# Kernel tuning notes

Measured on AMD Instinct MI355X. Metric: run time of the kernel, lower is better.

Reference implementation:

```python
import jax, jax.numpy as jnp
import numpy as np

D_MODEL = 512
D_STATE = 64
DT = 1.0
BATCH = 8
SEQ = 4096


def setup_inputs() -> dict:
    key = jax.random.key(0)
    ks = jax.random.split(key, 5)
    u = jax.random.normal(ks[0], (BATCH, SEQ, D_MODEL), dtype=jnp.float32)
    log_A_real = jnp.zeros((D_STATE,), dtype=jnp.float32)
    log_A_imag = 0.1 * jax.random.normal(ks[1], (D_STATE,), dtype=jnp.float32)
    B_w = 0.1 * jax.random.normal(ks[2], (2 * D_STATE, D_MODEL), dtype=jnp.float32)
    C_w = 0.1 * jax.random.normal(ks[3], (D_MODEL, 2 * D_STATE), dtype=jnp.float32)
    D_w = jnp.eye(D_MODEL, dtype=jnp.float32)
    return {"u": u, "log_A_real": log_A_real, "log_A_imag": log_A_imag,
            "B_w": B_w, "C_w": C_w, "D_w": D_w}


def reference(u, log_A_real, log_A_imag, B_w, C_w, D_w):
    # Bilinear discretization of diagonal A_c = -exp(log_A_real) + i*log_A_imag
    ar = -jnp.exp(log_A_real)
    ai = log_A_imag
    h = 0.5 * DT
    nr, ni = 1.0 + h * ar, h * ai          # numerator 1 + dt/2 * A
    dr, di = 1.0 - h * ar, -h * ai          # denominator 1 - dt/2 * A
    den = dr * dr + di * di
    Ar = (nr * dr + ni * di) / den          # Re(A_bar), shape (N,)
    Ai = (ni * dr - nr * di) / den          # Im(A_bar)

    N = log_A_real.shape[0]
    Bu = jnp.einsum('btd,nd->btn', u, B_w)  # (B, T, 2N)
    bu_re = jnp.swapaxes(Bu[..., :N], 0, 1)  # (T, B, N)
    bu_im = jnp.swapaxes(Bu[..., N:], 0, 1)

    batch = u.shape[0]
    h0 = (jnp.zeros((batch, N), u.dtype), jnp.zeros((batch, N), u.dtype))

    def step(carry, x):
        hr, hi = carry
        xr, xi = x
        nhr = Ar * hr - Ai * hi + xr        # complex multiply + add, real form
        nhi = Ar * hi + Ai * hr + xi
        return (nhr, nhi), (nhr, nhi)

    _, (hr_all, hi_all) = jax.lax.scan(step, h0, (bu_re, bu_im))
    h_cat = jnp.concatenate([hr_all, hi_all], axis=-1)   # (T, B, 2N)
    y = jnp.einsum('tbn,dn->btd', h_cat, C_w) + jnp.einsum('btd,ed->bte', u, D_w)
    return y
```

## Files before the change

### kernel.cpp

```cpp
#include <hip/hip_runtime.h>
#include <hip/hip_bf16.h>


#define D_MODEL 512
#define NSTATE  64
#define N2      128
#define BATCH   8
#define SEQ     4096
#define MTOT    (BATCH*SEQ)
#define LC      16
#define NC      (SEQ/LC)

#define OFFB_ABAR   0u
#define OFFB_POWTAB 512u
#define OFFB_BWPB   16384u
#define OFFB_W2B    147456u
#define OFFB_BU     1048576u
#define OFFB_E      17825792u
#define OFFB_P      18874368u

typedef __bf16  bf16x8  __attribute__((ext_vector_type(8)));
typedef float   f32x4   __attribute__((ext_vector_type(4)));
typedef unsigned short ushort8 __attribute__((ext_vector_type(8)));

__device__ __forceinline__ unsigned short f2bf(float f) {
    union { float f; unsigned int u; } v; v.f = f;
    unsigned int r = v.u + 0x7fffu + ((v.u >> 16) & 1u);
    return (unsigned short)(r >> 16);
}

__device__ __forceinline__ void gload_lds16(const void* g, void* l) {
    __builtin_amdgcn_global_load_lds(
        (const __attribute__((address_space(1))) void*)g,
        (__attribute__((address_space(3))) void*)l, 16, 0, 0);
}

__global__ __launch_bounds__(256) void prep_kernel(
    const float* __restrict__ lar, const float* __restrict__ lai,
    const float* __restrict__ Bw,  const float* __restrict__ Cw,
    const float* __restrict__ Dw,
    float* __restrict__ abar, float* __restrict__ powtab,
    unsigned short* __restrict__ Bwpb, unsigned short* __restrict__ W2b)
{
    int tid = blockIdx.x * blockDim.x + threadIdx.x;
    if (blockIdx.x == 0 && threadIdx.x < 64) {
        int n = threadIdx.x;
        float ar = -expf(lar[n]);
        float ai = lai[n];
        const float h = 0.5f;
        float nr = 1.f + h * ar, ni = h * ai;
        float dr = 1.f - h * ar, di = -h * ai;
        float den = dr * dr + di * di;
        float Ar = (nr * dr + ni * di) / den;
        float Ai = (ni * dr - nr * di) / den;
        abar[2 * n] = Ar; abar[2 * n + 1] = Ai;
        float pr = Ar, pi = Ai;
        for (int i = 0; i < LC; ++i) {
            powtab[(i * 64 + n) * 2]     = pr;
            powtab[(i * 64 + n) * 2 + 1] = pi;
            float npr = pr * Ar - pi * Ai;
            float npi = pr * Ai + pi * Ar;
            pr = npr; pi = npi;
        }
    }
    int stride = gridDim.x * blockDim.x;
    for (int idx = tid; idx < N2 * D_MODEL; idx += stride) {
        int np = idx / D_MODEL, k = idx % D_MODEL;
        int src = (np & 1) ? (64 + (np >> 1)) : (np >> 1);
        Bwpb[idx] = f2bf(Bw[src * D_MODEL + k]);
    }
    for (int idx = tid; idx < D_MODEL * 640; idx += stride) {
        int d = idx / 640, k = idx % 640;
        float v;
        if (k < D_MODEL) v = Dw[d * D_MODEL + k];
        else {
            int np = k - D_MODEL;
            int src = (np & 1) ? (64 + (np >> 1)) : (np >> 1);
            v = Cw[d * N2 + src];
        }
        W2b[idx] = f2bf(v);
    }
}

__global__ __launch_bounds__(256) void gemm_bf16_kernel(
    const float* __restrict__ A1, int lda1, int K1,
    const float* __restrict__ A2, int lda2, int K2,
    const unsigned short* __restrict__ W, int ldb,
    float* __restrict__ C, int ldc)
{
    __shared__ __align__(16) unsigned short As[128 * 64];
    __shared__ __align__(16) unsigned short Bs[128 * 64];
    const int tid  = threadIdx.x;
    const int lane = tid & 63;
    const int w    = tid >> 6;
    const int wm   = (w >> 1) * 64;
    const int wn   = (w & 1) * 64;
    const int m0   = blockIdx.x * 128;
    const int n0   = blockIdx.y * 128;

    f32x4 acc[4][4];
#pragma unroll
    for (int i = 0; i < 4; ++i)
#pragma unroll
        for (int j = 0; j < 4; ++j)
            acc[i][j] = (f32x4){0.f, 0.f, 0.f, 0.f};

    const int Ktot = K1 + K2;
    const int tr = tid >> 3;
    const int tc = tid & 7;

    for (int k0 = 0; k0 < Ktot; k0 += 64) {
        __syncthreads();
#pragma unroll
        for (int q = 0; q < 4; ++q) {
            int r = q * 32 + tr;
            int cs = tc ^ (r & 7);
            gload_lds16(W + (size_t)(n0 + r) * ldb + k0 + cs * 8,
                        (char*)Bs + (q * 256 + tid) * 16);
        }
        const float* Ab; int lda_; int kk0;
        if (k0 < K1) { Ab = A1; lda_ = lda1; kk0 = k0; }
        else         { Ab = A2; lda_ = lda2; kk0 = k0 - K1; }
#pragma unroll
        for (int q = 0; q < 4; ++q) {
            int r = q * 32 + tr;
            const float* src = Ab + (size_t)(m0 + r) * lda_ + kk0 + tc * 8;
            float4 v0 = *(const float4*)src;
            float4 v1 = *(const float4*)(src + 4);
            ushort8 p;
            p[0] = f2bf(v0.x); p[1] = f2bf(v0.y); p[2] = f2bf(v0.z); p[3] = f2bf(v0.w);
            p[4] = f2bf(v1.x); p[5] = f2bf(v1.y); p[6] = f2bf(v1.z); p[7] = f2bf(v1.w);
            int cd = tc ^ (r & 7);
            *(ushort8*)((char*)As + r * 128 + cd * 16) = p;
        }
        __syncthreads();

#pragma unroll
        for (int kk = 0; kk < 2; ++kk) {
            bf16x8 a[4], b[4];
#pragma unroll
            for (int i = 0; i < 4; ++i) {
                int row = wm + i * 16 + (lane & 15);
                int kb  = kk * 64 + ((lane >> 4) << 4);
                a[i] = *(const bf16x8*)((const char*)As + row * 128 + (kb ^ ((row & 7) << 4)));
            }
#pragma unroll
            for (int j = 0; j < 4; ++j) {
                int row = wn + j * 16 + (lane & 15);
                int kb  = kk * 64 + ((lane >> 4) << 4);
                b[j] = *(const bf16x8*)((const char*)Bs + row * 128 + (kb ^ ((row & 7) << 4)));
            }
#pragma unroll
            for (int i = 0; i < 4; ++i)
#pragma unroll
                for (int j = 0; j < 4; ++j)
                    acc[i][j] = __builtin_amdgcn_mfma_f32_16x16x32_bf16(a[i], b[j], acc[i][j], 0, 0, 0);
        }
    }

#pragma unroll
    for (int i = 0; i < 4; ++i)
#pragma unroll
        for (int j = 0; j < 4; ++j) {
            int col = n0 + wn + j * 16 + (lane & 15);
#pragma unroll
            for (int r = 0; r < 4; ++r) {
                int row = m0 + wm + i * 16 + ((lane >> 4) << 2) + r;
                C[(size_t)row * ldc + col] = acc[i][j][r];
            }
        }
}

__global__ __launch_bounds__(64) void scan_local_kernel(
    float* Bu, const float* __restrict__ abar, float* __restrict__ E)
{
    int n = threadIdx.x;
    int bx = blockIdx.x;
    int b = bx >> 8, c = bx & (NC - 1);
    float Ar = abar[2 * n], Ai = abar[2 * n + 1];
    float hr = 0.f, hi = 0.f;
    size_t base = (size_t)(b * SEQ + c * LC) * N2 + 2 * n;
#pragma unroll
    for (int i = 0; i < LC; ++i) {
        float2 x = *(const float2*)&Bu[base + (size_t)i * N2];
        float nhr = fmaf(Ar, hr, fmaf(-Ai, hi, x.x));
        float nhi = fmaf(Ar, hi, fmaf(Ai, hr, x.y));
        hr = nhr; hi = nhi;
        *(float2*)&Bu[base + (size_t)i * N2] = make_float2(hr, hi);
    }
    *(float2*)&E[((b * NC + c) * 64 + n) * 2] = make_float2(hr, hi);
}

__global__ __launch_bounds__(64) void scan_carry_kernel(
    const float* __restrict__ E, const float* __restrict__ powtab,
    float* __restrict__ P)
{
    int n = threadIdx.x;
    int b = blockIdx.x;
    float aLr = powtab[((LC - 1) * 64 + n) * 2];
    float aLi = powtab[((LC - 1) * 64 + n) * 2 + 1];
    float pr = 0.f, pi = 0.f;
    for (int c = 0; c < NC; ++c) {
        int idx = ((b * NC + c) * 64 + n) * 2;
        P[idx] = pr; P[idx + 1] = pi;
        float2 e = *(const float2*)&E[idx];
        float npr = fmaf(aLr, pr, fmaf(-aLi, pi, e.x));
        float npi = fmaf(aLr, pi, fmaf(aLi, pr, e.y));
        pr = npr; pi = npi;
    }
}

__global__ __launch_bounds__(64) void scan_fix_kernel(
    float* Bu, const float* __restrict__ P, const float* __restrict__ powtab)
{
    int n = threadIdx.x;
    int bx = blockIdx.x;
    int b = bx >> 8, c = bx & (NC - 1);
    if (c == 0) return;
    float2 p = *(const float2*)&P[((b * NC + c) * 64 + n) * 2];
    size_t base = (size_t)(b * SEQ + c * LC) * N2 + 2 * n;
#pragma unroll
    for (int i = 0; i < LC; ++i) {
        float2 wv = *(const float2*)&powtab[(i * 64 + n) * 2];
        float cr = wv.x * p.x - wv.y * p.y;
        float ci = fmaf(wv.x, p.y, wv.y * p.x);
        float2 hcur = *(const float2*)&Bu[base + (size_t)i * N2];
        hcur.x += cr; hcur.y += ci;
        *(float2*)&Bu[base + (size_t)i * N2] = hcur;
    }
}

extern "C" void kernel_launch(void* const* d_in, const int* in_sizes, int n_in,
                              void* d_out, int out_size, void* d_ws, size_t ws_size,
                              hipStream_t stream)
{
    const float* u   = (const float*)d_in[0];
    const float* lar = (const float*)d_in[1];
    const float* lai = (const float*)d_in[2];
    const float* Bw  = (const float*)d_in[3];
    const float* Cw  = (const float*)d_in[4];
    const float* Dw  = (const float*)d_in[5];
    float* y = (float*)d_out;
    char* ws = (char*)d_ws;

    float*          abar   = (float*)(ws + OFFB_ABAR);
    float*          powtab = (float*)(ws + OFFB_POWTAB);
    unsigned short* Bwpb   = (unsigned short*)(ws + OFFB_BWPB);
    unsigned short* W2b    = (unsigned short*)(ws + OFFB_W2B);
    float*          Bu     = (float*)(ws + OFFB_BU);
    float*          E      = (float*)(ws + OFFB_E);
    float*          P      = (float*)(ws + OFFB_P);

    hipLaunchKernelGGL(prep_kernel, dim3(128), dim3(256), 0, stream,
                       lar, lai, Bw, Cw, Dw, abar, powtab, Bwpb, W2b);
    hipLaunchKernelGGL(gemm_bf16_kernel, dim3(MTOT / 128, 1), dim3(256), 0, stream,
                       u, D_MODEL, D_MODEL, u, 0, 0, Bwpb, D_MODEL, Bu, N2);
    hipLaunchKernelGGL(scan_local_kernel, dim3(BATCH * NC), dim3(64), 0, stream,
                       Bu, abar, E);
    hipLaunchKernelGGL(scan_carry_kernel, dim3(BATCH), dim3(64), 0, stream,
                       E, powtab, P);
    hipLaunchKernelGGL(scan_fix_kernel, dim3(BATCH * NC), dim3(64), 0, stream,
                       Bu, P, powtab);
    hipLaunchKernelGGL(gemm_bf16_kernel, dim3(MTOT / 128, D_MODEL / 128), dim3(256), 0, stream,
                       u, D_MODEL, D_MODEL, Bu, N2, N2, W2b, 640, y, D_MODEL);
}
```

Before: 202.8 us.

## Fuse local scan into first GEMM, parallelize carry scan, apply fix in second GEMM

The first GEMM now computes Bu per 64-row tile, runs the 16-step local chunk scan in shared memory, and writes the local states as bf16 plus per-chunk end states. The carry scan is parallelized with a wave-level shuffle prefix scan over chunks instead of a serial loop. The carry correction (powtab times P) is applied inside the second GEMM's A-tile load, so the separate scan_local and scan_fix passes over the full fp32 Bu buffer go away. When the workspace is large enough, a bf16 copy of u is also cached so the second GEMM can load it directly with global-to-LDS copies instead of converting it again; this adds extra writes in the first GEMM and stores the local states in bf16.

```diff
diff --git a/kernel.cpp b/kernel.cpp
--- a/kernel.cpp
+++ b/kernel.cpp
@@ -3,21 +3,23 @@
 
 
 #define D_MODEL 512
-#define NSTATE  64
 #define N2      128
 #define BATCH   8
 #define SEQ     4096
 #define MTOT    (BATCH*SEQ)
 #define LC      16
 #define NC      (SEQ/LC)
+#define PADW    132
 
 #define OFFB_ABAR   0u
 #define OFFB_POWTAB 512u
 #define OFFB_BWPB   16384u
 #define OFFB_W2B    147456u
-#define OFFB_BU     1048576u
-#define OFFB_E      17825792u
-#define OFFB_P      18874368u
+#define OFFB_E      1048576u
+#define OFFB_P      2097152u
+#define OFFB_HLOC   3145728u
+#define OFFB_UBF    11534336u
+#define WS_NEED_UBF 45088768u
 
 typedef __bf16  bf16x8  __attribute__((ext_vector_type(8)));
 typedef float   f32x4   __attribute__((ext_vector_type(4)));
@@ -28,7 +30,10 @@
     unsigned int r = v.u + 0x7fffu + ((v.u >> 16) & 1u);
     return (unsigned short)(r >> 16);
 }
-
+__device__ __forceinline__ float bf2f(unsigned short s) {
+    union { unsigned int u; float f; } v; v.u = ((unsigned int)s) << 16;
+    return v.f;
+}
 __device__ __forceinline__ void gload_lds16(const void* g, void* l) {
     __builtin_amdgcn_global_load_lds(
         (const __attribute__((address_space(1))) void*)g,
@@ -56,8 +61,8 @@
         abar[2 * n] = Ar; abar[2 * n + 1] = Ai;
         float pr = Ar, pi = Ai;
         for (int i = 0; i < LC; ++i) {
-            powtab[(i * 64 + n) * 2]     = pr;
-            powtab[(i * 64 + n) * 2 + 1] = pi;
+            powtab[i * 128 + 2 * n]     = pr;
+            powtab[i * 128 + 2 * n + 1] = pi;
             float npr = pr * Ar - pi * Ai;
             float npi = pr * Ai + pi * Ar;
             pr = npr; pi = npi;
@@ -82,11 +87,193 @@
     }
 }
 
-__global__ __launch_bounds__(256) void gemm_bf16_kernel(
-    const float* __restrict__ A1, int lda1, int K1,
-    const float* __restrict__ A2, int lda2, int K2,
-    const unsigned short* __restrict__ W, int ldb,
-    float* __restrict__ C, int ldc)
+__global__ __launch_bounds__(256) void gemm1_fused(
+    const float* __restrict__ u, const unsigned short* __restrict__ Bwpb,
+    const float* __restrict__ abar,
+    unsigned short* __restrict__ Hloc, float* __restrict__ E,
+    unsigned short* __restrict__ u_bf, int write_ubf)
+{
+    __shared__ __align__(16) unsigned short As[64 * 64];
+    __shared__ __align__(16) unsigned short Bs[128 * 64];
+    __shared__ __align__(16) float Hs[64 * PADW];
+    const int tid  = threadIdx.x;
+    const int lane = tid & 63;
+    const int w    = tid >> 6;
+    const int wm   = (w >> 1) * 32;
+    const int wn   = (w & 1) * 64;
+    const int m0   = blockIdx.x * 64;
+
+    f32x4 acc[2][4];
+#pragma unroll
+    for (int i = 0; i < 2; ++i)
+#pragma unroll
+        for (int j = 0; j < 4; ++j)
+            acc[i][j] = (f32x4){0.f, 0.f, 0.f, 0.f};
+
+    const int tr = tid >> 3, tc = tid & 7;
+
+    for (int k0 = 0; k0 < D_MODEL; k0 += 64) {
+        __syncthreads();
+#pragma unroll
+        for (int q = 0; q < 4; ++q) {
+            int r = q * 32 + tr;
+            int cs = tc ^ (r & 7);
+            gload_lds16(Bwpb + (size_t)r * D_MODEL + k0 + cs * 8,
+                        (char*)Bs + (q * 256 + tid) * 16);
+        }
+#pragma unroll
+        for (int q = 0; q < 2; ++q) {
+            int r = q * 32 + tr;
+            const float* src = u + (size_t)(m0 + r) * D_MODEL + k0 + tc * 8;
+            float4 v0 = *(const float4*)src;
+            float4 v1 = *(const float4*)(src + 4);
+            ushort8 p;
+            p[0] = f2bf(v0.x); p[1] = f2bf(v0.y); p[2] = f2bf(v0.z); p[3] = f2bf(v0.w);
+            p[4] = f2bf(v1.x); p[5] = f2bf(v1.y); p[6] = f2bf(v1.z); p[7] = f2bf(v1.w);
+            int cd = tc ^ (r & 7);
+            *(ushort8*)((char*)As + r * 128 + cd * 16) = p;
+            if (write_ubf)
+                *(ushort8*)&u_bf[(size_t)(m0 + r) * D_MODEL + k0 + tc * 8] = p;
+        }
+        __syncthreads();
+#pragma unroll
+        for (int kk = 0; kk < 2; ++kk) {
+            bf16x8 a[2], b[4];
+#pragma unroll
+            for (int i = 0; i < 2; ++i) {
+                int row = wm + i * 16 + (lane & 15);
+                int kb  = kk * 64 + ((lane >> 4) << 4);
+                a[i] = *(const bf16x8*)((const char*)As + row * 128 + (kb ^ ((row & 7) << 4)));
+            }
+#pragma unroll
+            for (int j = 0; j < 4; ++j) {
+                int row = wn + j * 16 + (lane & 15);
+                int kb  = kk * 64 + ((lane >> 4) << 4);
+                b[j] = *(const bf16x8*)((const char*)Bs + row * 128 + (kb ^ ((row & 7) << 4)));
+            }
+#pragma unroll
+            for (int i = 0; i < 2; ++i)
+#pragma unroll
+                for (int j = 0; j < 4; ++j)
+                    acc[i][j] = __builtin_amdgcn_mfma_f32_16x16x32_bf16(a[i], b[j], acc[i][j], 0, 0, 0);
+        }
+    }
+
+#pragma unroll
+    for (int i = 0; i < 2; ++i)
+#pragma unroll
+        for (int j = 0; j < 4; ++j) {
+            int col = wn + j * 16 + (lane & 15);
+#pragma unroll
+            for (int r = 0; r < 4; ++r) {
+                int row = wm + i * 16 + ((lane >> 4) << 2) + r;
+                Hs[row * PADW + col] = acc[i][j][r];
+            }
+        }
+    __syncthreads();
+
+    {
+        int n  = tid & 63;
+        int cl = tid >> 6;
+        float2 ab = *(const float2*)&abar[2 * n];
+        float hr = 0.f, hi = 0.f;
+#pragma unroll
+        for (int i = 0; i < LC; ++i) {
+            int t = cl * LC + i;
+            float xr = Hs[t * PADW + 2 * n];
+            float xi = Hs[t * PADW + 2 * n + 1];
+            float nhr = fmaf(ab.x, hr, fmaf(-ab.y, hi, xr));
+            float nhi = fmaf(ab.x, hi, fmaf(ab.y, hr, xi));
+            hr = nhr; hi = nhi;
+            Hs[t * PADW + 2 * n]     = hr;
+            Hs[t * PADW + 2 * n + 1] = hi;
+        }
+        int b  = m0 >> 12;
+        int c0 = (m0 & 4095) >> 4;
+        *(float2*)&E[((size_t)(b * 64 + n) * NC + c0 + cl) * 2] = make_float2(hr, hi);
+    }
+    __syncthreads();
+
+#pragma unroll
+    for (int q = 0; q < 2; ++q) {
+        int r = q * 32 + tr;
+        int cb = tc * 16;
+        const float* row = &Hs[r * PADW + cb];
+        ushort8 o0, o1;
+#pragma unroll
+        for (int j = 0; j < 8; ++j) o0[j] = f2bf(row[j]);
+#pragma unroll
+        for (int j = 0; j < 8; ++j) o1[j] = f2bf(row[8 + j]);
+        *(ushort8*)&Hloc[(size_t)(m0 + r) * N2 + cb]     = o0;
+        *(ushort8*)&Hloc[(size_t)(m0 + r) * N2 + cb + 8] = o1;
+    }
+}
+
+__global__ __launch_bounds__(256) void scan_carry_par(
+    const float* __restrict__ E, const float* __restrict__ abar,
+    float* __restrict__ P)
+{
+    const int b    = blockIdx.x;
+    const int wv   = threadIdx.x >> 6;
+    const int lane = threadIdx.x & 63;
+
+    for (int n = wv * 16; n < wv * 16 + 16; ++n) {
+        float2 ab = *(const float2*)&abar[2 * n];
+        float ar = ab.x, ai = ab.y;
+        for (int k = 0; k < 4; ++k) {
+            float t = ar * ar - ai * ai;  ai = 2.f * ar * ai;  ar = t;
+        }
+        float pr[7], pi[7];
+        pr[0] = ar; pi[0] = ai;
+#pragma unroll
+        for (int k = 1; k < 7; ++k) {
+            pr[k] = pr[k-1] * pr[k-1] - pi[k-1] * pi[k-1];
+            pi[k] = 2.f * pr[k-1] * pi[k-1];
+        }
+        int L = lane + 1;
+        float wr = 1.f, wi = 0.f;
+#pragma unroll
+        for (int k = 0; k < 7; ++k) if ((L >> k) & 1) {
+            float t = wr * pr[k] - wi * pi[k];
+            wi = wr * pi[k] + wi * pr[k]; wr = t;
+        }
+        const float* Eb = E + (size_t)(b * 64 + n) * NC * 2;
+        float cr = 0.f, ci = 0.f;
+        for (int s = 0; s < 4; ++s) {
+            float2 e = *(const float2*)&Eb[(s * 64 + lane) * 2];
+            float xr = e.x, xi = e.y;
+#pragma unroll
+            for (int k = 0; k < 6; ++k) {
+                int d = 1 << k;
+                float tr_ = __shfl_up(xr, (unsigned)d);
+                float ti_ = __shfl_up(xi, (unsigned)d);
+                if (lane >= d) {
+                    xr = fmaf(pr[k], tr_, fmaf(-pi[k], ti_, xr));
+                    xi = fmaf(pr[k], ti_, fmaf(pi[k], tr_, xi));
+                }
+            }
+            float gr = fmaf(wr, cr, fmaf(-wi, ci, xr));
+            float gi = fmaf(wr, ci, fmaf(wi, cr, xi));
+            float exr = __shfl_up(gr, 1u);
+            float exi = __shfl_up(gi, 1u);
+            if (lane == 0) { exr = cr; exi = ci; }
+            *(float2*)&P[(size_t)(b * NC + s * 64 + lane) * N2 + 2 * n] =
+                make_float2(exr, exi);
+            cr = __shfl(gr, 63);
+            ci = __shfl(gi, 63);
+        }
+    }
+}
+
+template<bool A1BF>
+__global__ __launch_bounds__(256) void gemm2_fused(
+    const float* __restrict__ uf,
+    const unsigned short* __restrict__ ubf,
+    const unsigned short* __restrict__ Hloc,
+    const unsigned short* __restrict__ W2b,
+    const float* __restrict__ P,
+    const float* __restrict__ powtab,
+    float* __restrict__ y)
 {
     __shared__ __align__(16) unsigned short As[128 * 64];
     __shared__ __align__(16) unsigned short Bs[128 * 64];
@@ -105,36 +292,69 @@
         for (int j = 0; j < 4; ++j)
             acc[i][j] = (f32x4){0.f, 0.f, 0.f, 0.f};
 
-    const int Ktot = K1 + K2;
-    const int tr = tid >> 3;
-    const int tc = tid & 7;
-
-    for (int k0 = 0; k0 < Ktot; k0 += 64) {
+    const int tr = tid >> 3, tc = tid & 7;
+
+    for (int k0 = 0; k0 < 640; k0 += 64) {
         __syncthreads();
 #pragma unroll
         for (int q = 0; q < 4; ++q) {
             int r = q * 32 + tr;
             int cs = tc ^ (r & 7);
-            gload_lds16(W + (size_t)(n0 + r) * ldb + k0 + cs * 8,
+            gload_lds16(W2b + (size_t)(n0 + r) * 640 + k0 + cs * 8,
                         (char*)Bs + (q * 256 + tid) * 16);
         }
-        const float* Ab; int lda_; int kk0;
-        if (k0 < K1) { Ab = A1; lda_ = lda1; kk0 = k0; }
-        else         { Ab = A2; lda_ = lda2; kk0 = k0 - K1; }
-#pragma unroll
-        for (int q = 0; q < 4; ++q) {
-            int r = q * 32 + tr;
-            const float* src = Ab + (size_t)(m0 + r) * lda_ + kk0 + tc * 8;
-            float4 v0 = *(const float4*)src;
-            float4 v1 = *(const float4*)(src + 4);
-            ushort8 p;
-            p[0] = f2bf(v0.x); p[1] = f2bf(v0.y); p[2] = f2bf(v0.z); p[3] = f2bf(v0.w);
-            p[4] = f2bf(v1.x); p[5] = f2bf(v1.y); p[6] = f2bf(v1.z); p[7] = f2bf(v1.w);
-            int cd = tc ^ (r & 7);
-            *(ushort8*)((char*)As + r * 128 + cd * 16) = p;
+        if (k0 < D_MODEL) {
+            if constexpr (A1BF) {
+#pragma unroll
+                for (int q = 0; q < 4; ++q) {
+                    int r = q * 32 + tr;
+                    int cs = tc ^ (r & 7);
+                    gload_lds16(ubf + (size_t)(m0 + r) * D_MODEL + k0 + cs * 8,
+                                (char*)As + (q * 256 + tid) * 16);
+                }
+            } else {
+#pragma unroll
+                for (int q = 0; q < 4; ++q) {
+                    int r = q * 32 + tr;
+                    const float* src = uf + (size_t)(m0 + r) * D_MODEL + k0 + tc * 8;
+                    float4 v0 = *(const float4*)src;
+                    float4 v1 = *(const float4*)(src + 4);
+                    ushort8 p;
+                    p[0] = f2bf(v0.x); p[1] = f2bf(v0.y); p[2] = f2bf(v0.z); p[3] = f2bf(v0.w);
+                    p[4] = f2bf(v1.x); p[5] = f2bf(v1.y); p[6] = f2bf(v1.z); p[7] = f2bf(v1.w);
+                    int cd = tc ^ (r & 7);
+                    *(ushort8*)((char*)As + r * 128 + cd * 16) = p;
+                }
+            }
+        } else {
+            const int kk0 = k0 - D_MODEL;
+#pragma unroll
+            for (int q = 0; q < 4; ++q) {
+                int r = q * 32 + tr;
+                int m = m0 + r;
+                int b = m >> 12, t = m & 4095;
+                int c = t >> 4, i = t & 15;
+                ushort8 hl = *(const ushort8*)&Hloc[(size_t)m * N2 + kk0 + tc * 8];
+                const float* Pp = P + (size_t)(b * NC + c) * N2 + kk0 + tc * 8;
+                float4 p0 = *(const float4*)Pp;
+                float4 p1 = *(const float4*)(Pp + 4);
+                const float* Wp = powtab + i * 128 + kk0 + tc * 8;
+                float4 w0 = *(const float4*)Wp;
+                float4 w1 = *(const float4*)(Wp + 4);
+                ushort8 p;
+                p[0] = f2bf(fmaf(w0.x, p0.x, fmaf(-w0.y, p0.y, bf2f(hl[0]))));
+                p[1] = f2bf(fmaf(w0.x, p0.y, fmaf( w0.y, p0.x, bf2f(hl[1]))));
+                p[2] = f2bf(fmaf(w0.z, p0.z, fmaf(-w0.w, p0.w, bf2f(hl[2]))));
+                p[3] = f2bf(fmaf(w0.z, p0.w, fmaf( w0.w, p0.z, bf2f(hl[3]))));
+                p[4] = f2bf(fmaf(w1.x, p1.x, fmaf(-w1.y, p1.y, bf2f(hl[4]))));
+                p[5] = f2bf(fmaf(w1.x, p1.y, fmaf( w1.y, p1.x, bf2f(hl[5]))));
+                p[6] = f2bf(fmaf(w1.z, p1.z, fmaf(-w1.w, p1.w, bf2f(hl[6]))));
+                p[7] = f2bf(fmaf(w1.z, p1.w, fmaf( w1.w, p1.z, bf2f(hl[7]))));
+                int cd = tc ^ (r & 7);
+                *(ushort8*)((char*)As + r * 128 + cd * 16) = p;
+            }
         }
         __syncthreads();
-
 #pragma unroll
         for (int kk = 0; kk < 2; ++kk) {
             bf16x8 a[4], b[4];
@@ -166,68 +386,9 @@
 #pragma unroll
             for (int r = 0; r < 4; ++r) {
                 int row = m0 + wm + i * 16 + ((lane >> 4) << 2) + r;
-                C[(size_t)row * ldc + col] = acc[i][j][r];
-            }
-        }
-}
-
-__global__ __launch_bounds__(64) void scan_local_kernel(
-    float* Bu, const float* __restrict__ abar, float* __restrict__ E)
-{
-    int n = threadIdx.x;
-    int bx = blockIdx.x;
-    int b = bx >> 8, c = bx & (NC - 1);
-    float Ar = abar[2 * n], Ai = abar[2 * n + 1];
-    float hr = 0.f, hi = 0.f;
-    size_t base = (size_t)(b * SEQ + c * LC) * N2 + 2 * n;
-#pragma unroll
-    for (int i = 0; i < LC; ++i) {
-        float2 x = *(const float2*)&Bu[base + (size_t)i * N2];
-        float nhr = fmaf(Ar, hr, fmaf(-Ai, hi, x.x));
-        float nhi = fmaf(Ar, hi, fmaf(Ai, hr, x.y));
-        hr = nhr; hi = nhi;
-        *(float2*)&Bu[base + (size_t)i * N2] = make_float2(hr, hi);
-    }
-    *(float2*)&E[((b * NC + c) * 64 + n) * 2] = make_float2(hr, hi);
-}
-
-__global__ __launch_bounds__(64) void scan_carry_kernel(
-    const float* __restrict__ E, const float* __restrict__ powtab,
-    float* __restrict__ P)
-{
-    int n = threadIdx.x;
-    int b = blockIdx.x;
-    float aLr = powtab[((LC - 1) * 64 + n) * 2];
-    float aLi = powtab[((LC - 1) * 64 + n) * 2 + 1];
-    float pr = 0.f, pi = 0.f;
-    for (int c = 0; c < NC; ++c) {
-        int idx = ((b * NC + c) * 64 + n) * 2;
-        P[idx] = pr; P[idx + 1] = pi;
-        float2 e = *(const float2*)&E[idx];
-        float npr = fmaf(aLr, pr, fmaf(-aLi, pi, e.x));
-        float npi = fmaf(aLr, pi, fmaf(aLi, pr, e.y));
-        pr = npr; pi = npi;
-    }
-}
-
-__global__ __launch_bounds__(64) void scan_fix_kernel(
-    float* Bu, const float* __restrict__ P, const float* __restrict__ powtab)
-{
-    int n = threadIdx.x;
-    int bx = blockIdx.x;
-    int b = bx >> 8, c = bx & (NC - 1);
-    if (c == 0) return;
-    float2 p = *(const float2*)&P[((b * NC + c) * 64 + n) * 2];
-    size_t base = (size_t)(b * SEQ + c * LC) * N2 + 2 * n;
-#pragma unroll
-    for (int i = 0; i < LC; ++i) {
-        float2 wv = *(const float2*)&powtab[(i * 64 + n) * 2];
-        float cr = wv.x * p.x - wv.y * p.y;
-        float ci = fmaf(wv.x, p.y, wv.y * p.x);
-        float2 hcur = *(const float2*)&Bu[base + (size_t)i * N2];
-        hcur.x += cr; hcur.y += ci;
-        *(float2*)&Bu[base + (size_t)i * N2] = hcur;
-    }
+                y[(size_t)row * D_MODEL + col] = acc[i][j][r];
+            }
+        }
 }
 
 extern "C" void kernel_launch(void* const* d_in, const int* in_sizes, int n_in,
@@ -247,20 +408,26 @@
     float*          powtab = (float*)(ws + OFFB_POWTAB);
     unsigned short* Bwpb   = (unsigned short*)(ws + OFFB_BWPB);
     unsigned short* W2b    = (unsigned short*)(ws + OFFB_W2B);
-    float*          Bu     = (float*)(ws + OFFB_BU);
     float*          E      = (float*)(ws + OFFB_E);
     float*          P      = (float*)(ws + OFFB_P);
+    unsigned short* Hloc   = (unsigned short*)(ws + OFFB_HLOC);
+    unsigned short* u_bf   = (unsigned short*)(ws + OFFB_UBF);
+
+    const int use_ubf = (ws_size >= (size_t)WS_NEED_UBF) ? 1 : 0;
 
     hipLaunchKernelGGL(prep_kernel, dim3(128), dim3(256), 0, stream,
                        lar, lai, Bw, Cw, Dw, abar, powtab, Bwpb, W2b);
-    hipLaunchKernelGGL(gemm_bf16_kernel, dim3(MTOT / 128, 1), dim3(256), 0, stream,
-                       u, D_MODEL, D_MODEL, u, 0, 0, Bwpb, D_MODEL, Bu, N2);
-    hipLaunchKernelGGL(scan_local_kernel, dim3(BATCH * NC), dim3(64), 0, stream,
-                       Bu, abar, E);
-    hipLaunchKernelGGL(scan_carry_kernel, dim3(BATCH), dim3(64), 0, stream,
-                       E, powtab, P);
-    hipLaunchKernelGGL(scan_fix_kernel, dim3(BATCH * NC), dim3(64), 0, stream,
-                       Bu, P, powtab);
-    hipLaunchKernelGGL(gemm_bf16_kernel, dim3(MTOT / 128, D_MODEL / 128), dim3(256), 0, stream,
-                       u, D_MODEL, D_MODEL, Bu, N2, N2, W2b, 640, y, D_MODEL);
-}
+    hipLaunchKernelGGL(gemm1_fused, dim3(MTOT / 64), dim3(256), 0, stream,
+                       u, Bwpb, abar, Hloc, E, u_bf, use_ubf);
+    hipLaunchKernelGGL(scan_carry_par, dim3(BATCH), dim3(256), 0, stream,
+                       E, abar, P);
+    if (use_ubf) {
+        hipLaunchKernelGGL((gemm2_fused<true>), dim3(MTOT / 128, D_MODEL / 128),
+                           dim3(256), 0, stream,
+                           u, u_bf, Hloc, W2b, P, powtab, y);
+    } else {
+        hipLaunchKernelGGL((gemm2_fused<false>), dim3(MTOT / 128, D_MODEL / 128),
+                           dim3(256), 0, stream,
+                           u, u_bf, Hloc, W2b, P, powtab, y);
+    }
+}
```

Result: faster. 185.7 us (-8.4%).
